# Kernel tuning notes

Measured on AMD Instinct MI355X. Metric: run time of the kernel, lower is better.

The kernel has to match this reference:

```python
import jax, jax.numpy as jnp
import numpy as np
from functools import partial

B, DIN, H, D, HW = 4096, 2048, 1024, 256, 256
MAX_STEPS = 15
STEP = 1.0 / MAX_STEPS
WEIGHT = 1.0


def safe_norm(x):
    # per-sample L2 norm, keepdims, nan-safe at 0
    return jnp.sqrt(jnp.sum(x * x, axis=-1, keepdims=True) + 1e-24)


def setup_inputs() -> dict:
    key = jax.random.key(0)
    ks = jax.random.split(key, 16)
    s = lambda fan: 1.0 / np.sqrt(fan)
    inp = {
        'x_start': jax.random.normal(ks[0], (B, DIN), jnp.float32),
        'x_end': jax.random.normal(ks[1], (B, DIN), jnp.float32),
        'noise_raw': jax.random.normal(ks[2], (B, D), jnp.float32),
        # encoder params
        'W1': jax.random.normal(ks[3], (DIN, H), jnp.float32) * s(DIN),
        'b1': jnp.zeros((H,), jnp.float32),
        'W2': jax.random.normal(ks[4], (H, D), jnp.float32) * s(H),
        'b2': jnp.zeros((D,), jnp.float32),
        # Zermelo wind field params
        'Ww1': jax.random.normal(ks[5], (D, HW), jnp.float32) * s(D),
        'bw1': jnp.zeros((HW,), jnp.float32),
        'Ww2': jax.random.normal(ks[6], (HW, D), jnp.float32) * s(HW),
        'bw2': jnp.zeros((D,), jnp.float32),
        # conformal potential phi params (metric g = exp(phi) I)
        'Wp1': jax.random.normal(ks[7], (D, HW), jnp.float32) * s(D),
        'bp1': jnp.zeros((HW,), jnp.float32),
        'wp2': jax.random.normal(ks[8], (HW,), jnp.float32) * s(HW),
    }
    return inp


def _encode(x, W1, b1, W2, b2):
    return jnp.tanh(x @ W1 + b1) @ W2 + b2  # [B, D]


def _wind(z, Ww1, bw1, Ww2, bw2):
    return jnp.tanh(z @ Ww1 + bw1) @ Ww2 + bw2  # [B, D]


def _grad_phi(x, Wp1, bp1, wp2):
    # phi(x) = wp2 . tanh(x @ Wp1 + bp1); analytic gradient, fully vectorized
    h = jnp.tanh(x @ Wp1 + bp1)          # [B, HW]
    return ((1.0 - h * h) * wp2) @ Wp1.T  # [B, D]


def _accel(x, v, Wp1, bp1, wp2):
    # geodesic spray of conformal metric e^{phi} I:
    # a = -(grad_phi . v) v + 0.5 |v|^2 grad_phi
    g = _grad_phi(x, Wp1, bp1, wp2)
    gv = jnp.sum(g * v, axis=-1, keepdims=True)
    vv = jnp.sum(v * v, axis=-1, keepdims=True)
    return -gv * v + 0.5 * vv * g


def _trace(z0, v0, Wp1, bp1, wp2):
    h = STEP
    acc = partial(_accel, Wp1=Wp1, bp1=bp1, wp2=wp2)

    def step(carry, _):
        x, v = carry
        k1x, k1v = v, acc(x, v)
        k2x, k2v = v + 0.5 * h * k1v, acc(x + 0.5 * h * k1x, v + 0.5 * h * k1v)
        k3x, k3v = v + 0.5 * h * k2v, acc(x + 0.5 * h * k2x, v + 0.5 * h * k2v)
        k4x, k4v = v + h * k3v, acc(x + h * k3x, v + h * k3v)
        xn = x + (h / 6.0) * (k1x + 2 * k2x + 2 * k3x + k4x)
        vn = v + (h / 6.0) * (k1v + 2 * k2v + 2 * k3v + k4v)
        return (xn, vn), xn

    (_, _), xs = jax.lax.scan(step, (z0, v0), None, length=MAX_STEPS)
    return xs  # [MAX_STEPS, B, D] == xs[1:] of the original trace


def reference(x_start, x_end, noise_raw, W1, b1, W2, b2,
              Ww1, bw1, Ww2, bw2, Wp1, bp1, wp2):
    z_s = _encode(x_start, W1, b1, W2, b2)
    z_e = _encode(x_end, W1, b1, W2, b2)
    W_start = _wind(z_s, Ww1, bw1, Ww2, bw2)
    # degenerate-wind fallback: tiny tangent noise (Euclidean manifold -> identity projection)
    noise = noise_raw / (safe_norm(noise_raw) + 1e-12) * 1e-4
    w_norm = safe_norm(W_start)  # [B, 1]
    W_start = jnp.where(w_norm < 1e-5, W_start + noise, W_start)
    xs = _trace(z_s, W_start, Wp1, bp1, wp2)          # [S, B, D]
    dists_sq = jnp.sum((xs - z_e) ** 2, axis=-1)      # [S, B]
    min_dist_sq = jnp.min(dists_sq, axis=0)           # closest approach per sample
    return jnp.mean(min_dist_sq) * WEIGHT
```

## Files before the change

### kernel.cpp

```cpp
#include <hip/hip_runtime.h>
#include <math.h>

typedef short bf8 __attribute__((ext_vector_type(8)));
typedef float f32x4 __attribute__((ext_vector_type(4)));

namespace {

constexpr float H_STEP = 1.0f / 15.0f;

__device__ inline short f2bf(float f) {
  unsigned u = __float_as_uint(f);
  u += 0x7fffu + ((u >> 16) & 1u);
  return (short)(u >> 16);
}

__device__ inline float fast_tanh(float x) {
  const float ax = fabsf(x);
  const float e = __expf(-2.0f * ax);
  const float t = (1.0f - e) * __builtin_amdgcn_rcpf(1.0f + e);
  return copysignf(t, x);
}

__device__ inline float wave_sum(float v) {
#pragma unroll
  for (int sh = 32; sh > 0; sh >>= 1) v += __shfl_xor(v, sh);
  return v;
}

template <int CTRL>
__device__ inline float dppadd(float v) {
  return v + __int_as_float(__builtin_amdgcn_update_dpp(
                 0, __float_as_int(v), CTRL, 0xF, 0xF, true));
}
__device__ inline float red16(float v) {
  v = dppadd<0x121>(v);
  v = dppadd<0x122>(v);
  v = dppadd<0x124>(v);
  v = dppadd<0x128>(v);
  return v;
}

__device__ inline void async16(const void* g, void* l) {
  __builtin_amdgcn_global_load_lds((__attribute__((address_space(1))) void*)g,
                                   (__attribute__((address_space(3))) void*)l,
                                   16, 0, 0);
}


__global__ __launch_bounds__(256) void cvt2(const float* __restrict__ a,
                                            const float* __restrict__ b,
                                            short* __restrict__ dst, long n) {
  const long half = n >> 1;
  long i = ((long)blockIdx.x * 256 + threadIdx.x) * 4;
  const long stride = (long)gridDim.x * 1024;
  for (; i < n; i += stride) {
    const float* s = (i < half) ? (a + i) : (b + (i - half));
    const float4 f = *(const float4*)s;
    ushort4 o;
    o.x = (unsigned short)f2bf(f.x);
    o.y = (unsigned short)f2bf(f.y);
    o.z = (unsigned short)f2bf(f.z);
    o.w = (unsigned short)f2bf(f.w);
    *(ushort4*)(dst + i) = o;
  }
}

__global__ __launch_bounds__(256) void cvt_t(const float* __restrict__ src,
                                             short* __restrict__ dst, int K,
                                             int N) {
  __shared__ float tile[32][33];
  const int k0 = blockIdx.y * 32, n0 = blockIdx.x * 32;
  const int tr = threadIdx.x >> 5, tc = threadIdx.x & 31;
#pragma unroll
  for (int i = 0; i < 32; i += 8)
    tile[tr + i][tc] = src[(size_t)(k0 + tr + i) * N + n0 + tc];
  __syncthreads();
#pragma unroll
  for (int i = 0; i < 32; i += 8)
    dst[(size_t)(n0 + tr + i) * K + k0 + tc] = f2bf(tile[tc][tr + i]);
}

__global__ __launch_bounds__(256) void cvt4(const float* __restrict__ Ww1,
                                            const float* __restrict__ Ww2,
                                            const float* __restrict__ Wp1,
                                            short* __restrict__ d0,
                                            short* __restrict__ d1,
                                            short* __restrict__ d2,
                                            short* __restrict__ d3) {
  __shared__ float tile[32][33];
  const int z = blockIdx.z;
  const int k0 = blockIdx.y * 32, n0 = blockIdx.x * 32;
  const int tr = threadIdx.x >> 5, tc = threadIdx.x & 31;
  if (z == 3) {
#pragma unroll
    for (int i = 0; i < 32; i += 8) {
      const size_t o = (size_t)(k0 + tr + i) * 256 + n0 + tc;
      d3[o] = f2bf(Wp1[o]);
    }
    return;
  }
  const float* src = (z == 0) ? Ww1 : (z == 1) ? Ww2 : Wp1;
  short* dst = (z == 0) ? d0 : (z == 1) ? d1 : d2;
#pragma unroll
  for (int i = 0; i < 32; i += 8)
    tile[tr + i][tc] = src[(size_t)(k0 + tr + i) * 256 + n0 + tc];
  __syncthreads();
#pragma unroll
  for (int i = 0; i < 32; i += 8)
    dst[(size_t)(n0 + tr + i) * 256 + k0 + tc] = f2bf(tile[tc][tr + i]);
}


enum { EPI_TANH = 0, EPI_F32 = 1, EPI_ENC2 = 2 };

template <int EPI>
__global__ __launch_bounds__(256) void gemm128(
    const short* __restrict__ A, const short* __restrict__ Bt,
    const float* __restrict__ bias, float* __restrict__ Cf,
    short* __restrict__ Cb, int M, int N, int K) {
  __shared__ __align__(16) short As[128 * 32];
  __shared__ __align__(16) short Bs[128 * 32];
  const int tid = threadIdx.x;
  const int w = tid >> 6, lane = tid & 63, q = lane >> 4, l15 = lane & 15;
  const int wm = (w >> 1) * 64, wn = (w & 1) * 64;
  const int m0 = blockIdx.y * 128, n0 = blockIdx.x * 128;
  const f32x4 fzero = {0.0f, 0.0f, 0.0f, 0.0f};
  f32x4 acc[4][4];
#pragma unroll
  for (int mt = 0; mt < 4; ++mt)
#pragma unroll
    for (int nt = 0; nt < 4; ++nt) acc[mt][nt] = fzero;

  for (int k0 = 0; k0 < K; k0 += 32) {
#pragma unroll
    for (int j = 0; j < 2; ++j) {
      const int c = w * 128 + j * 64 + lane;
      async16(A + (size_t)(m0 + (c >> 2)) * K + k0 + (c & 3) * 8,
              &As[(w * 128 + j * 64) * 8]);
      async16(Bt + (size_t)(n0 + (c >> 2)) * K + k0 + (c & 3) * 8,
              &Bs[(w * 128 + j * 64) * 8]);
    }
    __syncthreads();
    bf8 af[4], bfr[4];
#pragma unroll
    for (int mt = 0; mt < 4; ++mt)
      af[mt] = *(const bf8*)&As[(wm + mt * 16 + l15) * 32 + q * 8];
#pragma unroll
    for (int nt = 0; nt < 4; ++nt)
      bfr[nt] = *(const bf8*)&Bs[(wn + nt * 16 + l15) * 32 + q * 8];
#pragma unroll
    for (int mt = 0; mt < 4; ++mt)
#pragma unroll
      for (int nt = 0; nt < 4; ++nt)
        acc[mt][nt] = __builtin_amdgcn_mfma_f32_16x16x32_bf16(
            af[mt], bfr[nt], acc[mt][nt], 0, 0, 0);
    __syncthreads();
  }
#pragma unroll
  for (int mt = 0; mt < 4; ++mt)
#pragma unroll
    for (int nt = 0; nt < 4; ++nt) {
      const int col = n0 + wn + nt * 16 + l15;
      const float bcol = bias[col];
#pragma unroll
      for (int rg = 0; rg < 4; ++rg) {
        const int row = m0 + wm + mt * 16 + q * 4 + rg;
        const float val = acc[mt][nt][rg] + bcol;
        if constexpr (EPI == EPI_TANH) {
          Cb[(size_t)row * N + col] = f2bf(fast_tanh(val));
        } else {
          Cf[(size_t)row * N + col] = val;
        }
      }
    }
}

template <int EPI>
__global__ __launch_bounds__(256) void gemm64(
    const short* __restrict__ A, const short* __restrict__ Bt,
    const float* __restrict__ bias, float* __restrict__ Cf,
    short* __restrict__ Cb, float* __restrict__ Cf2, int M, int N, int K) {
  __shared__ __align__(16) short As[64 * 32];
  __shared__ __align__(16) short Bs[64 * 32];
  const int tid = threadIdx.x;
  const int w = tid >> 6, lane = tid & 63, q = lane >> 4, l15 = lane & 15;
  const int wm = (w >> 1) * 32, wn = (w & 1) * 32;
  const int m0 = blockIdx.y * 64, n0 = blockIdx.x * 64;
  const f32x4 fzero = {0.0f, 0.0f, 0.0f, 0.0f};
  f32x4 acc[2][2];
#pragma unroll
  for (int mt = 0; mt < 2; ++mt)
#pragma unroll
    for (int nt = 0; nt < 2; ++nt) acc[mt][nt] = fzero;

  for (int k0 = 0; k0 < K; k0 += 32) {
    const int c = w * 64 + lane;
    async16(A + (size_t)(m0 + (c >> 2)) * K + k0 + (c & 3) * 8,
            &As[(w * 64) * 8]);
    async16(Bt + (size_t)(n0 + (c >> 2)) * K + k0 + (c & 3) * 8,
            &Bs[(w * 64) * 8]);
    __syncthreads();
    bf8 af[2], bfr[2];
#pragma unroll
    for (int mt = 0; mt < 2; ++mt)
      af[mt] = *(const bf8*)&As[(wm + mt * 16 + l15) * 32 + q * 8];
#pragma unroll
    for (int nt = 0; nt < 2; ++nt)
      bfr[nt] = *(const bf8*)&Bs[(wn + nt * 16 + l15) * 32 + q * 8];
#pragma unroll
    for (int mt = 0; mt < 2; ++mt)
#pragma unroll
      for (int nt = 0; nt < 2; ++nt)
        acc[mt][nt] = __builtin_amdgcn_mfma_f32_16x16x32_bf16(
            af[mt], bfr[nt], acc[mt][nt], 0, 0, 0);
    __syncthreads();
  }
#pragma unroll
  for (int mt = 0; mt < 2; ++mt)
#pragma unroll
    for (int nt = 0; nt < 2; ++nt) {
      const int col = n0 + wn + nt * 16 + l15;
      const float bcol = bias[col];
#pragma unroll
      for (int rg = 0; rg < 4; ++rg) {
        const int row = m0 + wm + mt * 16 + q * 4 + rg;
        const float val = acc[mt][nt][rg] + bcol;
        if constexpr (EPI == EPI_TANH) {
          Cb[(size_t)row * N + col] = f2bf(fast_tanh(val));
        } else if constexpr (EPI == EPI_F32) {
          Cf[(size_t)row * N + col] = val;
        } else {
          if (row < 4096) {
            Cf[(size_t)row * N + col] = val;
            Cb[(size_t)row * N + col] = f2bf(val);
          } else {
            Cf2[(size_t)(row - 4096) * N + col] = val;
          }
        }
      }
    }
}


__global__ __launch_bounds__(256) void init_fb(float* __restrict__ V,
                                               const float* __restrict__ nr) {
  const int row = blockIdx.x * 4 + (threadIdx.x >> 6);
  const int lane = threadIdx.x & 63;
  const size_t off = (size_t)row * 256 + (lane << 2);
  float4 wv = *(const float4*)(V + off);
  float s = wv.x * wv.x + wv.y * wv.y + wv.z * wv.z + wv.w * wv.w;
  s = wave_sum(s);
  const float wn = sqrtf(s + 1e-24f);
  if (wn < 1e-5f) {
    const float4 n4 = *(const float4*)(nr + off);
    float ns = n4.x * n4.x + n4.y * n4.y + n4.z * n4.z + n4.w * n4.w;
    ns = wave_sum(ns);
    const float nn = sqrtf(ns + 1e-24f);
    const float sc = 1e-4f / (nn + 1e-12f);
    wv.x += sc * n4.x; wv.y += sc * n4.y; wv.z += sc * n4.z; wv.w += sc * n4.w;
    *(float4*)(V + off) = wv;
  }
}


__global__ __launch_bounds__(512, 2) void trace_fused(
    const float* __restrict__ Xg, const float* __restrict__ Vg,
    const float* __restrict__ ZEg, const short* __restrict__ WT,
    const short* __restrict__ Wp1b, const float* __restrict__ bp1,
    const float* __restrict__ wp2, float* __restrict__ out) {
  constexpr float hs = H_STEP;
  __shared__ __align__(16) short XsL[4096];
  __shared__ __align__(16) short UL[4096];
  __shared__ __align__(16) float gvb[2][16];
  __shared__ __align__(16) float vvb[2][16];
  __shared__ __align__(16) float db[2][16];
  const int tid = threadIdx.x;
  const int w = tid >> 6, lane = tid & 63, q = lane >> 4, l15 = lane & 15;
  const int r0 = blockIdx.x * 16, rb = q * 4;

  if (tid < 16) {
    gvb[0][tid] = 0.0f; gvb[1][tid] = 0.0f;
    vvb[0][tid] = 0.0f; vvb[1][tid] = 0.0f;
    db[0][tid] = 0.0f;  db[1][tid] = 0.0f;
  }

  bf8 B1f[2][8], B2f[2][8];
  int wadr[2][4], radr[8];
  float bp1c[2], wp2c[2];
  float x[2][4], v[2][4], ap[2][4], xacc[2][4], vacc[2][4], ze[2][4], md[4];
#pragma unroll
  for (int t = 0; t < 2; ++t) {
    const int c = w * 32 + t * 16 + l15;
    const int kc = c >> 3, cx = kc & 15, cl = c & 7;
#pragma unroll
    for (int ks = 0; ks < 8; ++ks) {
      B1f[t][ks] = *(const bf8*)(WT + c * 256 + ks * 32 + q * 8);
      B2f[t][ks] = *(const bf8*)(Wp1b + c * 256 + ks * 32 + q * 8);
    }
    bp1c[t] = bp1[c];
    wp2c[t] = wp2[c];
#pragma unroll
    for (int rg = 0; rg < 4; ++rg) {
      wadr[t][rg] = kc * 128 + ((rb + rg) ^ cx) * 8 + cl;
      const size_t off = (size_t)(r0 + rb + rg) * 256 + c;
      x[t][rg] = Xg[off];
      v[t][rg] = Vg[off];
      ze[t][rg] = ZEg[off];
      ap[t][rg] = 0.0f;
      xacc[t][rg] = 0.0f;
      vacc[t][rg] = 0.0f;
    }
  }
#pragma unroll
  for (int ks = 0; ks < 8; ++ks) {
    const int kq = ks * 4 + q;
    radr[ks] = (kq * 16 + (l15 ^ (kq & 15))) * 8;
  }
#pragma unroll
  for (int rg = 0; rg < 4; ++rg) md[rg] = 3.4e38f;
  const f32x4 fzero = {0.0f, 0.0f, 0.0f, 0.0f};
  const float cxv_t[4] = {0.0f, 0.5f * hs, 0.5f * hs, hs};
  const float cxa_t[4] = {0.0f, 0.0f, 0.25f * hs * hs, 0.5f * hs * hs};
  const float cva_t[4] = {0.0f, 0.5f * hs, 0.5f * hs, hs};

#pragma unroll 1
  for (int step = 0; step < 15; ++step) {
#pragma unroll
    for (int st = 0; st < 4; ++st) {
      const int p = st & 1;
      const float cxv = cxv_t[st], cxa = cxa_t[st], cva = cva_t[st];
#pragma unroll
      for (int t = 0; t < 2; ++t)
#pragma unroll
        for (int rg = 0; rg < 4; ++rg)
          XsL[wadr[t][rg]] =
              f2bf(x[t][rg] + cxv * v[t][rg] + cxa * ap[t][rg]);
      __syncthreads();
      bf8 af[8];
#pragma unroll
      for (int ks = 0; ks < 8; ++ks) af[ks] = *(const bf8*)&XsL[radr[ks]];
      f32x4 acc[2];
#pragma unroll
      for (int t = 0; t < 2; ++t) {
        f32x4 a0 = fzero, a1 = fzero;
#pragma unroll
        for (int ks = 0; ks < 8; ks += 2) {
          a0 = __builtin_amdgcn_mfma_f32_16x16x32_bf16(af[ks], B1f[t][ks], a0,
                                                       0, 0, 0);
          a1 = __builtin_amdgcn_mfma_f32_16x16x32_bf16(af[ks + 1],
                                                       B1f[t][ks + 1], a1, 0,
                                                       0, 0);
        }
        acc[t] = a0 + a1;
      }
#pragma unroll
      for (int t = 0; t < 2; ++t)
#pragma unroll
        for (int rg = 0; rg < 4; ++rg) {
          const float th = fast_tanh(acc[t][rg] + bp1c[t]);
          UL[wadr[t][rg]] = f2bf((1.0f - th * th) * wp2c[t]);
        }
      if (tid < 16) {
        gvb[p ^ 1][tid] = 0.0f;
        vvb[p ^ 1][tid] = 0.0f;
      }
      __syncthreads();
#pragma unroll
      for (int ks = 0; ks < 8; ++ks) af[ks] = *(const bf8*)&UL[radr[ks]];
#pragma unroll
      for (int t = 0; t < 2; ++t) {
        f32x4 a0 = fzero, a1 = fzero;
#pragma unroll
        for (int ks = 0; ks < 8; ks += 2) {
          a0 = __builtin_amdgcn_mfma_f32_16x16x32_bf16(af[ks], B2f[t][ks], a0,
                                                       0, 0, 0);
          a1 = __builtin_amdgcn_mfma_f32_16x16x32_bf16(af[ks + 1],
                                                       B2f[t][ks + 1], a1, 0,
                                                       0, 0);
        }
        acc[t] = a0 + a1;
      }
      float pg[4] = {0, 0, 0, 0}, pv[4] = {0, 0, 0, 0};
#pragma unroll
      for (int t = 0; t < 2; ++t)
#pragma unroll
        for (int rg = 0; rg < 4; ++rg) {
          const float vs = fmaf(cva, ap[t][rg], v[t][rg]);
          pg[rg] = fmaf(acc[t][rg], vs, pg[rg]);
          pv[rg] = fmaf(vs, vs, pv[rg]);
        }
#pragma unroll
      for (int rg = 0; rg < 4; ++rg) {
        pg[rg] = red16(pg[rg]);
        pv[rg] = red16(pv[rg]);
      }
      if (l15 == 0) {
#pragma unroll
        for (int rg = 0; rg < 4; ++rg) {
          atomicAdd(&gvb[p][rb + rg], pg[rg]);
          atomicAdd(&vvb[p][rb + rg], pv[rg]);
        }
      }
      __syncthreads();
      const f32x4 gv4 = *(const f32x4*)&gvb[p][rb];
      const f32x4 vv4 = *(const f32x4*)&vvb[p][rb];
#pragma unroll
      for (int t = 0; t < 2; ++t)
#pragma unroll
        for (int rg = 0; rg < 4; ++rg) {
          const float vs = fmaf(cva, ap[t][rg], v[t][rg]);
          const float a = -gv4[rg] * vs + 0.5f * vv4[rg] * acc[t][rg];
          ap[t][rg] = a;
          if (st == 0) {
            xacc[t][rg] = a;
            vacc[t][rg] = a;
          } else if (st < 3) {
            xacc[t][rg] += a;
            vacc[t][rg] += 2.0f * a;
          } else {
            vacc[t][rg] += a;
          }
        }
      if (st == 3) {
        const int sp = step & 1;
        float pd[4] = {0, 0, 0, 0};
#pragma unroll
        for (int t = 0; t < 2; ++t)
#pragma unroll
          for (int rg = 0; rg < 4; ++rg) {
            const float xn =
                x[t][rg] + hs * v[t][rg] + (hs * hs / 6.0f) * xacc[t][rg];
            const float vn = v[t][rg] + (hs / 6.0f) * vacc[t][rg];
            x[t][rg] = xn;
            v[t][rg] = vn;
            const float d = xn - ze[t][rg];
            pd[rg] = fmaf(d, d, pd[rg]);
          }
#pragma unroll
        for (int rg = 0; rg < 4; ++rg) pd[rg] = red16(pd[rg]);
        if (l15 == 0) {
#pragma unroll
          for (int rg = 0; rg < 4; ++rg) atomicAdd(&db[sp][rb + rg], pd[rg]);
        }
        if (tid < 16) db[sp ^ 1][tid] = 0.0f;
        __syncthreads();
        const f32x4 d4 = *(const f32x4*)&db[sp][rb];
#pragma unroll
        for (int rg = 0; rg < 4; ++rg) md[rg] = fminf(md[rg], d4[rg]);
      }
    }
  }
  if (w == 0 && l15 == 0)
    atomicAdd(out, (md[0] + md[1] + md[2] + md[3]) * (1.0f / 4096.0f));
}

}

extern "C" void kernel_launch(void* const* d_in, const int* in_sizes, int n_in,
                              void* d_out, int out_size, void* d_ws,
                              size_t ws_size, hipStream_t stream) {
  (void)in_sizes; (void)n_in; (void)out_size; (void)ws_size;
  const float* x_start = (const float*)d_in[0];
  const float* x_end = (const float*)d_in[1];
  const float* noise = (const float*)d_in[2];
  const float* W1 = (const float*)d_in[3];
  const float* b1 = (const float*)d_in[4];
  const float* W2 = (const float*)d_in[5];
  const float* b2 = (const float*)d_in[6];
  const float* Ww1 = (const float*)d_in[7];
  const float* bw1 = (const float*)d_in[8];
  const float* Ww2 = (const float*)d_in[9];
  const float* bw2 = (const float*)d_in[10];
  const float* Wp1 = (const float*)d_in[11];
  const float* bp1 = (const float*)d_in[12];
  const float* wp2 = (const float*)d_in[13];
  float* out = (float*)d_out;

  float* Xf = (float*)d_ws;
  float* ZEf = Xf + (size_t)4096 * 256;
  float* Vf = ZEf + (size_t)4096 * 256;
  short* Xb = (short*)(Vf + (size_t)4096 * 256);
  short* HWb = Xb + (size_t)4096 * 256;
  short* XSb = HWb + (size_t)4096 * 256;
  short* H1b = XSb + (size_t)8192 * 2048;
  short* W1T = H1b + (size_t)8192 * 1024;
  short* W2T = W1T + (size_t)1024 * 2048;
  short* Ww1T = W2T + (size_t)256 * 1024;
  short* Ww2T = Ww1T + 65536;
  short* WpT = Ww2T + 65536;
  short* Wp1b = WpT + 65536;

  const dim3 blk(256);

  cvt_t<<<dim3(32, 64), blk, 0, stream>>>(W1, W1T, 2048, 1024);
  cvt_t<<<dim3(8, 32), blk, 0, stream>>>(W2, W2T, 1024, 256);
  cvt4<<<dim3(8, 8, 4), blk, 0, stream>>>(Ww1, Ww2, Wp1, Ww1T, Ww2T, WpT,
                                          Wp1b);
  cvt2<<<2048, blk, 0, stream>>>(x_start, x_end, XSb, (long)8192 * 2048);
  gemm128<EPI_TANH><<<dim3(8, 64), blk, 0, stream>>>(
      XSb, W1T, b1, nullptr, H1b, 8192, 1024, 2048);
  gemm64<EPI_ENC2><<<dim3(4, 128), blk, 0, stream>>>(
      H1b, W2T, b2, Xf, Xb, ZEf, 8192, 256, 1024);
  gemm64<EPI_TANH><<<dim3(4, 64), blk, 0, stream>>>(
      Xb, Ww1T, bw1, nullptr, HWb, nullptr, 4096, 256, 256);
  gemm64<EPI_F32><<<dim3(4, 64), blk, 0, stream>>>(
      HWb, Ww2T, bw2, Vf, nullptr, nullptr, 4096, 256, 256);
  init_fb<<<1024, blk, 0, stream>>>(Vf, noise);

  hipMemsetAsync(d_out, 0, sizeof(float), stream);
  trace_fused<<<256, dim3(512), 0, stream>>>(Xf, Vf, ZEf, WpT, Wp1b, bp1, wp2,
                                             out);
}
```

Baseline: 346.0 us.

## Widen trace kernel to 1024 threads, deepen GEMM K-tile, use sech2

The fused RK4 trace kernel now runs 16 waves per block, each owning one 16-column slice instead of two. This halves per-thread register state and raises the number of waves available to hide latency. The large encoder GEMM now loads two 32-wide K chunks per barrier pair, which halves the synchronisation count but doubles shared memory use. tanh-derivative is computed directly as sech^2 via one exp and one rcp. The risks are higher barrier cost across 1024 threads and register pressure under the new launch bounds.

```diff
diff --git a/kernel.cpp b/kernel.cpp
--- a/kernel.cpp
+++ b/kernel.cpp
@@ -19,6 +19,12 @@
   const float e = __expf(-2.0f * ax);
   const float t = (1.0f - e) * __builtin_amdgcn_rcpf(1.0f + e);
   return copysignf(t, x);
+}
+
+__device__ inline float sech2(float x) {
+  const float e = __expf(-2.0f * fabsf(x));
+  const float r = __builtin_amdgcn_rcpf(1.0f + e);
+  return 4.0f * e * r * r;
 }
 
 __device__ inline float wave_sum(float v) {
@@ -118,8 +124,8 @@
     const short* __restrict__ A, const short* __restrict__ Bt,
     const float* __restrict__ bias, float* __restrict__ Cf,
     short* __restrict__ Cb, int M, int N, int K) {
-  __shared__ __align__(16) short As[128 * 32];
-  __shared__ __align__(16) short Bs[128 * 32];
+  __shared__ __align__(16) short As[2 * 128 * 32];
+  __shared__ __align__(16) short Bs[2 * 128 * 32];
   const int tid = threadIdx.x;
   const int w = tid >> 6, lane = tid & 63, q = lane >> 4, l15 = lane & 15;
   const int wm = (w >> 1) * 64, wn = (w & 1) * 64;
@@ -131,29 +137,36 @@
 #pragma unroll
     for (int nt = 0; nt < 4; ++nt) acc[mt][nt] = fzero;
 
-  for (int k0 = 0; k0 < K; k0 += 32) {
-#pragma unroll
-    for (int j = 0; j < 2; ++j) {
-      const int c = w * 128 + j * 64 + lane;
-      async16(A + (size_t)(m0 + (c >> 2)) * K + k0 + (c & 3) * 8,
-              &As[(w * 128 + j * 64) * 8]);
-      async16(Bt + (size_t)(n0 + (c >> 2)) * K + k0 + (c & 3) * 8,
-              &Bs[(w * 128 + j * 64) * 8]);
-    }
+  for (int k0 = 0; k0 < K; k0 += 64) {
+#pragma unroll
+    for (int kcb = 0; kcb < 2; ++kcb)
+#pragma unroll
+      for (int j = 0; j < 2; ++j) {
+        const int c = w * 128 + j * 64 + lane;
+        async16(A + (size_t)(m0 + (c >> 2)) * K + k0 + kcb * 32 + (c & 3) * 8,
+                &As[kcb * 4096 + (w * 128 + j * 64) * 8]);
+        async16(Bt + (size_t)(n0 + (c >> 2)) * K + k0 + kcb * 32 + (c & 3) * 8,
+                &Bs[kcb * 4096 + (w * 128 + j * 64) * 8]);
+      }
     __syncthreads();
-    bf8 af[4], bfr[4];
-#pragma unroll
-    for (int mt = 0; mt < 4; ++mt)
-      af[mt] = *(const bf8*)&As[(wm + mt * 16 + l15) * 32 + q * 8];
-#pragma unroll
-    for (int nt = 0; nt < 4; ++nt)
-      bfr[nt] = *(const bf8*)&Bs[(wn + nt * 16 + l15) * 32 + q * 8];
-#pragma unroll
-    for (int mt = 0; mt < 4; ++mt)
+#pragma unroll
+    for (int kcb = 0; kcb < 2; ++kcb) {
+      bf8 af[4], bfr[4];
+#pragma unroll
+      for (int mt = 0; mt < 4; ++mt)
+        af[mt] =
+            *(const bf8*)&As[kcb * 4096 + (wm + mt * 16 + l15) * 32 + q * 8];
 #pragma unroll
       for (int nt = 0; nt < 4; ++nt)
-        acc[mt][nt] = __builtin_amdgcn_mfma_f32_16x16x32_bf16(
-            af[mt], bfr[nt], acc[mt][nt], 0, 0, 0);
+        bfr[nt] =
+            *(const bf8*)&Bs[kcb * 4096 + (wn + nt * 16 + l15) * 32 + q * 8];
+#pragma unroll
+      for (int mt = 0; mt < 4; ++mt)
+#pragma unroll
+        for (int nt = 0; nt < 4; ++nt)
+          acc[mt][nt] = __builtin_amdgcn_mfma_f32_16x16x32_bf16(
+              af[mt], bfr[nt], acc[mt][nt], 0, 0, 0);
+    }
     __syncthreads();
   }
 #pragma unroll
@@ -263,7 +276,7 @@
 }
 
 
-__global__ __launch_bounds__(512, 2) void trace_fused(
+__global__ __launch_bounds__(1024, 4) void trace_fused(
     const float* __restrict__ Xg, const float* __restrict__ Vg,
     const float* __restrict__ ZEg, const short* __restrict__ WT,
     const short* __restrict__ Wp1b, const float* __restrict__ bp1,
@@ -284,40 +297,39 @@
     db[0][tid] = 0.0f;  db[1][tid] = 0.0f;
   }
 
-  bf8 B1f[2][8], B2f[2][8];
-  int wadr[2][4], radr[8];
-  float bp1c[2], wp2c[2];
-  float x[2][4], v[2][4], ap[2][4], xacc[2][4], vacc[2][4], ze[2][4], md[4];
-#pragma unroll
-  for (int t = 0; t < 2; ++t) {
-    const int c = w * 32 + t * 16 + l15;
+  const int c = w * 16 + l15;
+  bf8 B1f[8], B2f[8];
+#pragma unroll
+  for (int ks = 0; ks < 8; ++ks) {
+    B1f[ks] = *(const bf8*)(WT + c * 256 + ks * 32 + q * 8);
+    B2f[ks] = *(const bf8*)(Wp1b + c * 256 + ks * 32 + q * 8);
+  }
+  const float bp1c = bp1[c];
+  const float wp2c = wp2[c];
+  int wadr[4], radr[8];
+  {
     const int kc = c >> 3, cx = kc & 15, cl = c & 7;
 #pragma unroll
+    for (int rg = 0; rg < 4; ++rg)
+      wadr[rg] = kc * 128 + ((rb + rg) ^ cx) * 8 + cl;
+#pragma unroll
     for (int ks = 0; ks < 8; ++ks) {
-      B1f[t][ks] = *(const bf8*)(WT + c * 256 + ks * 32 + q * 8);
-      B2f[t][ks] = *(const bf8*)(Wp1b + c * 256 + ks * 32 + q * 8);
-    }
-    bp1c[t] = bp1[c];
-    wp2c[t] = wp2[c];
-#pragma unroll
-    for (int rg = 0; rg < 4; ++rg) {
-      wadr[t][rg] = kc * 128 + ((rb + rg) ^ cx) * 8 + cl;
-      const size_t off = (size_t)(r0 + rb + rg) * 256 + c;
-      x[t][rg] = Xg[off];
-      v[t][rg] = Vg[off];
-      ze[t][rg] = ZEg[off];
-      ap[t][rg] = 0.0f;
-      xacc[t][rg] = 0.0f;
-      vacc[t][rg] = 0.0f;
-    }
-  }
-#pragma unroll
-  for (int ks = 0; ks < 8; ++ks) {
-    const int kq = ks * 4 + q;
-    radr[ks] = (kq * 16 + (l15 ^ (kq & 15))) * 8;
-  }
-#pragma unroll
-  for (int rg = 0; rg < 4; ++rg) md[rg] = 3.4e38f;
+      const int kq = ks * 4 + q;
+      radr[ks] = (kq * 16 + (l15 ^ (kq & 15))) * 8;
+    }
+  }
+  float x[4], v[4], ap[4], xacc[4], vacc[4], ze[4], md[4];
+#pragma unroll
+  for (int rg = 0; rg < 4; ++rg) {
+    const size_t off = (size_t)(r0 + rb + rg) * 256 + c;
+    x[rg] = Xg[off];
+    v[rg] = Vg[off];
+    ze[rg] = ZEg[off];
+    ap[rg] = 0.0f;
+    xacc[rg] = 0.0f;
+    vacc[rg] = 0.0f;
+    md[rg] = 3.4e38f;
+  }
   const f32x4 fzero = {0.0f, 0.0f, 0.0f, 0.0f};
   const float cxv_t[4] = {0.0f, 0.5f * hs, 0.5f * hs, hs};
   const float cxa_t[4] = {0.0f, 0.0f, 0.25f * hs * hs, 0.5f * hs * hs};
@@ -330,69 +342,50 @@
       const int p = st & 1;
       const float cxv = cxv_t[st], cxa = cxa_t[st], cva = cva_t[st];
 #pragma unroll
-      for (int t = 0; t < 2; ++t)
-#pragma unroll
-        for (int rg = 0; rg < 4; ++rg)
-          XsL[wadr[t][rg]] =
-              f2bf(x[t][rg] + cxv * v[t][rg] + cxa * ap[t][rg]);
+      for (int rg = 0; rg < 4; ++rg)
+        XsL[wadr[rg]] = f2bf(x[rg] + cxv * v[rg] + cxa * ap[rg]);
       __syncthreads();
-      bf8 af[8];
-#pragma unroll
-      for (int ks = 0; ks < 8; ++ks) af[ks] = *(const bf8*)&XsL[radr[ks]];
-      f32x4 acc[2];
-#pragma unroll
-      for (int t = 0; t < 2; ++t) {
+      f32x4 acc;
+      {
         f32x4 a0 = fzero, a1 = fzero;
 #pragma unroll
         for (int ks = 0; ks < 8; ks += 2) {
-          a0 = __builtin_amdgcn_mfma_f32_16x16x32_bf16(af[ks], B1f[t][ks], a0,
-                                                       0, 0, 0);
-          a1 = __builtin_amdgcn_mfma_f32_16x16x32_bf16(af[ks + 1],
-                                                       B1f[t][ks + 1], a1, 0,
+          const bf8 f0 = *(const bf8*)&XsL[radr[ks]];
+          const bf8 f1 = *(const bf8*)&XsL[radr[ks + 1]];
+          a0 = __builtin_amdgcn_mfma_f32_16x16x32_bf16(f0, B1f[ks], a0, 0, 0,
+                                                       0);
+          a1 = __builtin_amdgcn_mfma_f32_16x16x32_bf16(f1, B1f[ks + 1], a1, 0,
                                                        0, 0);
         }
-        acc[t] = a0 + a1;
-      }
-#pragma unroll
-      for (int t = 0; t < 2; ++t)
-#pragma unroll
-        for (int rg = 0; rg < 4; ++rg) {
-          const float th = fast_tanh(acc[t][rg] + bp1c[t]);
-          UL[wadr[t][rg]] = f2bf((1.0f - th * th) * wp2c[t]);
-        }
+        acc = a0 + a1;
+      }
+#pragma unroll
+      for (int rg = 0; rg < 4; ++rg)
+        UL[wadr[rg]] = f2bf(sech2(acc[rg] + bp1c) * wp2c);
       if (tid < 16) {
         gvb[p ^ 1][tid] = 0.0f;
         vvb[p ^ 1][tid] = 0.0f;
       }
       __syncthreads();
-#pragma unroll
-      for (int ks = 0; ks < 8; ++ks) af[ks] = *(const bf8*)&UL[radr[ks]];
-#pragma unroll
-      for (int t = 0; t < 2; ++t) {
+      {
         f32x4 a0 = fzero, a1 = fzero;
 #pragma unroll
         for (int ks = 0; ks < 8; ks += 2) {
-          a0 = __builtin_amdgcn_mfma_f32_16x16x32_bf16(af[ks], B2f[t][ks], a0,
-                                                       0, 0, 0);
-          a1 = __builtin_amdgcn_mfma_f32_16x16x32_bf16(af[ks + 1],
-                                                       B2f[t][ks + 1], a1, 0,
+          const bf8 f0 = *(const bf8*)&UL[radr[ks]];
+          const bf8 f1 = *(const bf8*)&UL[radr[ks + 1]];
+          a0 = __builtin_amdgcn_mfma_f32_16x16x32_bf16(f0, B2f[ks], a0, 0, 0,
+                                                       0);
+          a1 = __builtin_amdgcn_mfma_f32_16x16x32_bf16(f1, B2f[ks + 1], a1, 0,
                                                        0, 0);
         }
-        acc[t] = a0 + a1;
-      }
-      float pg[4] = {0, 0, 0, 0}, pv[4] = {0, 0, 0, 0};
-#pragma unroll
-      for (int t = 0; t < 2; ++t)
-#pragma unroll
-        for (int rg = 0; rg < 4; ++rg) {
-          const float vs = fmaf(cva, ap[t][rg], v[t][rg]);
-          pg[rg] = fmaf(acc[t][rg], vs, pg[rg]);
-          pv[rg] = fmaf(vs, vs, pv[rg]);
-        }
+        acc = a0 + a1;
+      }
+      float pg[4], pv[4];
 #pragma unroll
       for (int rg = 0; rg < 4; ++rg) {
-        pg[rg] = red16(pg[rg]);
-        pv[rg] = red16(pv[rg]);
+        const float vs = fmaf(cva, ap[rg], v[rg]);
+        pg[rg] = red16(acc[rg] * vs);
+        pv[rg] = red16(vs * vs);
       }
       if (l15 == 0) {
 #pragma unroll
@@ -405,39 +398,32 @@
       const f32x4 gv4 = *(const f32x4*)&gvb[p][rb];
       const f32x4 vv4 = *(const f32x4*)&vvb[p][rb];
 #pragma unroll
-      for (int t = 0; t < 2; ++t)
-#pragma unroll
-        for (int rg = 0; rg < 4; ++rg) {
-          const float vs = fmaf(cva, ap[t][rg], v[t][rg]);
-          const float a = -gv4[rg] * vs + 0.5f * vv4[rg] * acc[t][rg];
-          ap[t][rg] = a;
-          if (st == 0) {
-            xacc[t][rg] = a;
-            vacc[t][rg] = a;
-          } else if (st < 3) {
-            xacc[t][rg] += a;
-            vacc[t][rg] += 2.0f * a;
-          } else {
-            vacc[t][rg] += a;
-          }
-        }
+      for (int rg = 0; rg < 4; ++rg) {
+        const float vs = fmaf(cva, ap[rg], v[rg]);
+        const float a = -gv4[rg] * vs + 0.5f * vv4[rg] * acc[rg];
+        ap[rg] = a;
+        if (st == 0) {
+          xacc[rg] = a;
+          vacc[rg] = a;
+        } else if (st < 3) {
+          xacc[rg] += a;
+          vacc[rg] += 2.0f * a;
+        } else {
+          vacc[rg] += a;
+        }
+      }
       if (st == 3) {
         const int sp = step & 1;
-        float pd[4] = {0, 0, 0, 0};
-#pragma unroll
-        for (int t = 0; t < 2; ++t)
-#pragma unroll
-          for (int rg = 0; rg < 4; ++rg) {
-            const float xn =
-                x[t][rg] + hs * v[t][rg] + (hs * hs / 6.0f) * xacc[t][rg];
-            const float vn = v[t][rg] + (hs / 6.0f) * vacc[t][rg];
-            x[t][rg] = xn;
-            v[t][rg] = vn;
-            const float d = xn - ze[t][rg];
-            pd[rg] = fmaf(d, d, pd[rg]);
-          }
-#pragma unroll
-        for (int rg = 0; rg < 4; ++rg) pd[rg] = red16(pd[rg]);
+        float pd[4];
+#pragma unroll
+        for (int rg = 0; rg < 4; ++rg) {
+          const float xn = x[rg] + hs * v[rg] + (hs * hs / 6.0f) * xacc[rg];
+          const float vn = v[rg] + (hs / 6.0f) * vacc[rg];
+          x[rg] = xn;
+          v[rg] = vn;
+          const float d = xn - ze[rg];
+          pd[rg] = red16(d * d);
+        }
         if (l15 == 0) {
 #pragma unroll
           for (int rg = 0; rg < 4; ++rg) atomicAdd(&db[sp][rb + rg], pd[rg]);
@@ -508,6 +494,6 @@
   init_fb<<<1024, blk, 0, stream>>>(Vf, noise);
 
   hipMemsetAsync(d_out, 0, sizeof(float), stream);
-  trace_fused<<<256, dim3(512), 0, stream>>>(Xf, Vf, ZEf, WpT, Wp1b, bp1, wp2,
-                                             out);
-}
+  trace_fused<<<256, dim3(1024), 0, stream>>>(Xf, Vf, ZEf, WpT, Wp1b, bp1,
+                                              wp2, out);
+}
```

Result: slower. 381.8 us (+10.4%).

## Fuse wind MLP and fallback into trace kernel, merge weight conversions

Applied to the files above, without the earlier changes.

Moves the wind-field MLP (two small GEMMs) and the degenerate-wind noise fallback into the trace kernel, dropping three launches and the round trips of the bf16 Xb, HWb and V intermediates. All weight conversions are merged into one launch, and wp2 is folded into the bf16 Wp1 copy so the spray uses sech² directly. The big encoder GEMM now stages two K-chunks per barrier, halving its synchronisations. The catch is more register pressure and serial startup work inside the trace kernel, plus a larger LDS footprint in the GEMM.

```diff
diff --git a/kernel.cpp b/kernel.cpp
--- a/kernel.cpp
+++ b/kernel.cpp
@@ -19,6 +19,12 @@
   const float e = __expf(-2.0f * ax);
   const float t = (1.0f - e) * __builtin_amdgcn_rcpf(1.0f + e);
   return copysignf(t, x);
+}
+
+__device__ inline float sech2(float x) {
+  const float e = __expf(-2.0f * fabsf(x));
+  const float r = __builtin_amdgcn_rcpf(1.0f + e);
+  return 4.0f * e * r * r;
 }
 
 __device__ inline float wave_sum(float v) {
@@ -65,12 +71,40 @@
   }
 }
 
-__global__ __launch_bounds__(256) void cvt_t(const float* __restrict__ src,
-                                             short* __restrict__ dst, int K,
-                                             int N) {
+__global__ __launch_bounds__(256) void cvt_w(
+    const float* __restrict__ W1, const float* __restrict__ W2,
+    const float* __restrict__ Ww1, const float* __restrict__ Ww2,
+    const float* __restrict__ Wp1, const float* __restrict__ wp2,
+    short* __restrict__ W1T, short* __restrict__ W2T,
+    short* __restrict__ Ww1T, short* __restrict__ Ww2T,
+    short* __restrict__ WpT, short* __restrict__ Wp1s) {
   __shared__ float tile[32][33];
-  const int k0 = blockIdx.y * 32, n0 = blockIdx.x * 32;
+  const int id = blockIdx.x;
   const int tr = threadIdx.x >> 5, tc = threadIdx.x & 31;
+  const float* src;
+  short* dst;
+  int K, N, kt, nt;
+  if (id < 2048) {
+    src = W1; dst = W1T; K = 2048; N = 1024; kt = id >> 5; nt = id & 31;
+  } else if (id < 2304) {
+    src = W2; dst = W2T; K = 1024; N = 256; kt = (id - 2048) >> 3; nt = (id - 2048) & 7;
+  } else if (id < 2368) {
+    src = Ww1; dst = Ww1T; K = 256; N = 256; kt = (id - 2304) >> 3; nt = (id - 2304) & 7;
+  } else if (id < 2432) {
+    src = Ww2; dst = Ww2T; K = 256; N = 256; kt = (id - 2368) >> 3; nt = (id - 2368) & 7;
+  } else if (id < 2496) {
+    src = Wp1; dst = WpT; K = 256; N = 256; kt = (id - 2432) >> 3; nt = (id - 2432) & 7;
+  } else {
+    const int lid = id - 2496;
+    const int k0 = (lid >> 3) * 32, n0 = (lid & 7) * 32;
+#pragma unroll
+    for (int i = 0; i < 32; i += 8) {
+      const size_t o = (size_t)(k0 + tr + i) * 256 + n0 + tc;
+      Wp1s[o] = f2bf(Wp1[o] * wp2[n0 + tc]);
+    }
+    return;
+  }
+  const int k0 = kt * 32, n0 = nt * 32;
 #pragma unroll
   for (int i = 0; i < 32; i += 8)
     tile[tr + i][tc] = src[(size_t)(k0 + tr + i) * N + n0 + tc];
@@ -80,46 +114,13 @@
     dst[(size_t)(n0 + tr + i) * K + k0 + tc] = f2bf(tile[tc][tr + i]);
 }
 
-__global__ __launch_bounds__(256) void cvt4(const float* __restrict__ Ww1,
-                                            const float* __restrict__ Ww2,
-                                            const float* __restrict__ Wp1,
-                                            short* __restrict__ d0,
-                                            short* __restrict__ d1,
-                                            short* __restrict__ d2,
-                                            short* __restrict__ d3) {
-  __shared__ float tile[32][33];
-  const int z = blockIdx.z;
-  const int k0 = blockIdx.y * 32, n0 = blockIdx.x * 32;
-  const int tr = threadIdx.x >> 5, tc = threadIdx.x & 31;
-  if (z == 3) {
-#pragma unroll
-    for (int i = 0; i < 32; i += 8) {
-      const size_t o = (size_t)(k0 + tr + i) * 256 + n0 + tc;
-      d3[o] = f2bf(Wp1[o]);
-    }
-    return;
-  }
-  const float* src = (z == 0) ? Ww1 : (z == 1) ? Ww2 : Wp1;
-  short* dst = (z == 0) ? d0 : (z == 1) ? d1 : d2;
-#pragma unroll
-  for (int i = 0; i < 32; i += 8)
-    tile[tr + i][tc] = src[(size_t)(k0 + tr + i) * 256 + n0 + tc];
-  __syncthreads();
-#pragma unroll
-  for (int i = 0; i < 32; i += 8)
-    dst[(size_t)(n0 + tr + i) * 256 + k0 + tc] = f2bf(tile[tc][tr + i]);
-}
-
-
-enum { EPI_TANH = 0, EPI_F32 = 1, EPI_ENC2 = 2 };
-
-template <int EPI>
-__global__ __launch_bounds__(256) void gemm128(
+
+__global__ __launch_bounds__(256) void gemm128_tanh(
     const short* __restrict__ A, const short* __restrict__ Bt,
-    const float* __restrict__ bias, float* __restrict__ Cf,
-    short* __restrict__ Cb, int M, int N, int K) {
-  __shared__ __align__(16) short As[128 * 32];
-  __shared__ __align__(16) short Bs[128 * 32];
+    const float* __restrict__ bias, short* __restrict__ Cb, int M, int N,
+    int K) {
+  __shared__ __align__(16) short As[2 * 128 * 32];
+  __shared__ __align__(16) short Bs[2 * 128 * 32];
   const int tid = threadIdx.x;
   const int w = tid >> 6, lane = tid & 63, q = lane >> 4, l15 = lane & 15;
   const int wm = (w >> 1) * 64, wn = (w & 1) * 64;
@@ -131,29 +132,36 @@
 #pragma unroll
     for (int nt = 0; nt < 4; ++nt) acc[mt][nt] = fzero;
 
-  for (int k0 = 0; k0 < K; k0 += 32) {
-#pragma unroll
-    for (int j = 0; j < 2; ++j) {
-      const int c = w * 128 + j * 64 + lane;
-      async16(A + (size_t)(m0 + (c >> 2)) * K + k0 + (c & 3) * 8,
-              &As[(w * 128 + j * 64) * 8]);
-      async16(Bt + (size_t)(n0 + (c >> 2)) * K + k0 + (c & 3) * 8,
-              &Bs[(w * 128 + j * 64) * 8]);
-    }
-    __syncthreads();
-    bf8 af[4], bfr[4];
-#pragma unroll
-    for (int mt = 0; mt < 4; ++mt)
-      af[mt] = *(const bf8*)&As[(wm + mt * 16 + l15) * 32 + q * 8];
-#pragma unroll
-    for (int nt = 0; nt < 4; ++nt)
-      bfr[nt] = *(const bf8*)&Bs[(wn + nt * 16 + l15) * 32 + q * 8];
-#pragma unroll
-    for (int mt = 0; mt < 4; ++mt)
+  for (int k0 = 0; k0 < K; k0 += 64) {
+#pragma unroll
+    for (int kcb = 0; kcb < 2; ++kcb)
+#pragma unroll
+      for (int j = 0; j < 2; ++j) {
+        const int c = w * 128 + j * 64 + lane;
+        async16(A + (size_t)(m0 + (c >> 2)) * K + k0 + kcb * 32 + (c & 3) * 8,
+                &As[kcb * 4096 + (w * 128 + j * 64) * 8]);
+        async16(Bt + (size_t)(n0 + (c >> 2)) * K + k0 + kcb * 32 + (c & 3) * 8,
+                &Bs[kcb * 4096 + (w * 128 + j * 64) * 8]);
+      }
+    __syncthreads();
+#pragma unroll
+    for (int kcb = 0; kcb < 2; ++kcb) {
+      bf8 af[4], bfr[4];
+#pragma unroll
+      for (int mt = 0; mt < 4; ++mt)
+        af[mt] =
+            *(const bf8*)&As[kcb * 4096 + (wm + mt * 16 + l15) * 32 + q * 8];
 #pragma unroll
       for (int nt = 0; nt < 4; ++nt)
-        acc[mt][nt] = __builtin_amdgcn_mfma_f32_16x16x32_bf16(
-            af[mt], bfr[nt], acc[mt][nt], 0, 0, 0);
+        bfr[nt] =
+            *(const bf8*)&Bs[kcb * 4096 + (wn + nt * 16 + l15) * 32 + q * 8];
+#pragma unroll
+      for (int mt = 0; mt < 4; ++mt)
+#pragma unroll
+        for (int nt = 0; nt < 4; ++nt)
+          acc[mt][nt] = __builtin_amdgcn_mfma_f32_16x16x32_bf16(
+              af[mt], bfr[nt], acc[mt][nt], 0, 0, 0);
+    }
     __syncthreads();
   }
 #pragma unroll
@@ -165,21 +173,15 @@
 #pragma unroll
       for (int rg = 0; rg < 4; ++rg) {
         const int row = m0 + wm + mt * 16 + q * 4 + rg;
-        const float val = acc[mt][nt][rg] + bcol;
-        if constexpr (EPI == EPI_TANH) {
-          Cb[(size_t)row * N + col] = f2bf(fast_tanh(val));
-        } else {
-          Cf[(size_t)row * N + col] = val;
-        }
-      }
-    }
-}
-
-template <int EPI>
-__global__ __launch_bounds__(256) void gemm64(
+        Cb[(size_t)row * N + col] = f2bf(fast_tanh(acc[mt][nt][rg] + bcol));
+      }
+    }
+}
+
+__global__ __launch_bounds__(256) void gemm64_enc2(
     const short* __restrict__ A, const short* __restrict__ Bt,
-    const float* __restrict__ bias, float* __restrict__ Cf,
-    short* __restrict__ Cb, float* __restrict__ Cf2, int M, int N, int K) {
+    const float* __restrict__ bias, float* __restrict__ Zs,
+    float* __restrict__ Ze, int M, int N, int K) {
   __shared__ __align__(16) short As[64 * 32];
   __shared__ __align__(16) short Bs[64 * 32];
   const int tid = threadIdx.x;
@@ -225,49 +227,22 @@
       for (int rg = 0; rg < 4; ++rg) {
         const int row = m0 + wm + mt * 16 + q * 4 + rg;
         const float val = acc[mt][nt][rg] + bcol;
-        if constexpr (EPI == EPI_TANH) {
-          Cb[(size_t)row * N + col] = f2bf(fast_tanh(val));
-        } else if constexpr (EPI == EPI_F32) {
-          Cf[(size_t)row * N + col] = val;
-        } else {
-          if (row < 4096) {
-            Cf[(size_t)row * N + col] = val;
-            Cb[(size_t)row * N + col] = f2bf(val);
-          } else {
-            Cf2[(size_t)(row - 4096) * N + col] = val;
-          }
-        }
-      }
-    }
-}
-
-
-__global__ __launch_bounds__(256) void init_fb(float* __restrict__ V,
-                                               const float* __restrict__ nr) {
-  const int row = blockIdx.x * 4 + (threadIdx.x >> 6);
-  const int lane = threadIdx.x & 63;
-  const size_t off = (size_t)row * 256 + (lane << 2);
-  float4 wv = *(const float4*)(V + off);
-  float s = wv.x * wv.x + wv.y * wv.y + wv.z * wv.z + wv.w * wv.w;
-  s = wave_sum(s);
-  const float wn = sqrtf(s + 1e-24f);
-  if (wn < 1e-5f) {
-    const float4 n4 = *(const float4*)(nr + off);
-    float ns = n4.x * n4.x + n4.y * n4.y + n4.z * n4.z + n4.w * n4.w;
-    ns = wave_sum(ns);
-    const float nn = sqrtf(ns + 1e-24f);
-    const float sc = 1e-4f / (nn + 1e-12f);
-    wv.x += sc * n4.x; wv.y += sc * n4.y; wv.z += sc * n4.z; wv.w += sc * n4.w;
-    *(float4*)(V + off) = wv;
-  }
+        if (row < 4096)
+          Zs[(size_t)row * N + col] = val;
+        else
+          Ze[(size_t)(row - 4096) * N + col] = val;
+      }
+    }
 }
 
 
 __global__ __launch_bounds__(512, 2) void trace_fused(
-    const float* __restrict__ Xg, const float* __restrict__ Vg,
-    const float* __restrict__ ZEg, const short* __restrict__ WT,
-    const short* __restrict__ Wp1b, const float* __restrict__ bp1,
-    const float* __restrict__ wp2, float* __restrict__ out) {
+    const float* __restrict__ Xg, const float* __restrict__ ZEg,
+    const float* __restrict__ NZg, const short* __restrict__ WT,
+    const short* __restrict__ Wp1s, const short* __restrict__ Ww1T,
+    const short* __restrict__ Ww2T, const float* __restrict__ bw1,
+    const float* __restrict__ bw2, const float* __restrict__ bp1,
+    float* __restrict__ out) {
   constexpr float hs = H_STEP;
   __shared__ __align__(16) short XsL[4096];
   __shared__ __align__(16) short UL[4096];
@@ -284,41 +259,138 @@
     db[0][tid] = 0.0f;  db[1][tid] = 0.0f;
   }
 
-  bf8 B1f[2][8], B2f[2][8];
-  int wadr[2][4], radr[8];
-  float bp1c[2], wp2c[2];
-  float x[2][4], v[2][4], ap[2][4], xacc[2][4], vacc[2][4], ze[2][4], md[4];
+  int cc[2], wadr[2][4], radr[8];
+  float bp1c[2], bw1c[2], bw2c[2];
 #pragma unroll
   for (int t = 0; t < 2; ++t) {
     const int c = w * 32 + t * 16 + l15;
+    cc[t] = c;
     const int kc = c >> 3, cx = kc & 15, cl = c & 7;
 #pragma unroll
-    for (int ks = 0; ks < 8; ++ks) {
-      B1f[t][ks] = *(const bf8*)(WT + c * 256 + ks * 32 + q * 8);
-      B2f[t][ks] = *(const bf8*)(Wp1b + c * 256 + ks * 32 + q * 8);
-    }
+    for (int rg = 0; rg < 4; ++rg)
+      wadr[t][rg] = kc * 128 + ((rb + rg) ^ cx) * 8 + cl;
     bp1c[t] = bp1[c];
-    wp2c[t] = wp2[c];
-#pragma unroll
-    for (int rg = 0; rg < 4; ++rg) {
-      wadr[t][rg] = kc * 128 + ((rb + rg) ^ cx) * 8 + cl;
-      const size_t off = (size_t)(r0 + rb + rg) * 256 + c;
-      x[t][rg] = Xg[off];
-      v[t][rg] = Vg[off];
-      ze[t][rg] = ZEg[off];
-      ap[t][rg] = 0.0f;
-      xacc[t][rg] = 0.0f;
-      vacc[t][rg] = 0.0f;
-    }
+    bw1c[t] = bw1[c];
+    bw2c[t] = bw2[c];
   }
 #pragma unroll
   for (int ks = 0; ks < 8; ++ks) {
     const int kq = ks * 4 + q;
     radr[ks] = (kq * 16 + (l15 ^ (kq & 15))) * 8;
   }
-#pragma unroll
-  for (int rg = 0; rg < 4; ++rg) md[rg] = 3.4e38f;
+  float x[2][4], ze[2][4], nz[2][4];
+#pragma unroll
+  for (int t = 0; t < 2; ++t)
+#pragma unroll
+    for (int rg = 0; rg < 4; ++rg) {
+      const size_t off = (size_t)(r0 + rb + rg) * 256 + cc[t];
+      x[t][rg] = Xg[off];
+      ze[t][rg] = ZEg[off];
+      nz[t][rg] = NZg[off];
+    }
   const f32x4 fzero = {0.0f, 0.0f, 0.0f, 0.0f};
+
+  float v[2][4];
+  {
+    bf8 Wf1[2][8], Wf2[2][8];
+#pragma unroll
+    for (int t = 0; t < 2; ++t)
+#pragma unroll
+      for (int ks = 0; ks < 8; ++ks) {
+        Wf1[t][ks] = *(const bf8*)(Ww1T + cc[t] * 256 + ks * 32 + q * 8);
+        Wf2[t][ks] = *(const bf8*)(Ww2T + cc[t] * 256 + ks * 32 + q * 8);
+      }
+#pragma unroll
+    for (int t = 0; t < 2; ++t)
+#pragma unroll
+      for (int rg = 0; rg < 4; ++rg) XsL[wadr[t][rg]] = f2bf(x[t][rg]);
+    __syncthreads();
+    bf8 af[8];
+#pragma unroll
+    for (int ks = 0; ks < 8; ++ks) af[ks] = *(const bf8*)&XsL[radr[ks]];
+    f32x4 acc[2];
+#pragma unroll
+    for (int t = 0; t < 2; ++t) {
+      f32x4 a0 = fzero, a1 = fzero;
+#pragma unroll
+      for (int ks = 0; ks < 8; ks += 2) {
+        a0 = __builtin_amdgcn_mfma_f32_16x16x32_bf16(af[ks], Wf1[t][ks], a0,
+                                                     0, 0, 0);
+        a1 = __builtin_amdgcn_mfma_f32_16x16x32_bf16(af[ks + 1],
+                                                     Wf1[t][ks + 1], a1, 0, 0,
+                                                     0);
+      }
+      acc[t] = a0 + a1;
+    }
+#pragma unroll
+    for (int t = 0; t < 2; ++t)
+#pragma unroll
+      for (int rg = 0; rg < 4; ++rg)
+        UL[wadr[t][rg]] = f2bf(fast_tanh(acc[t][rg] + bw1c[t]));
+    __syncthreads();
+#pragma unroll
+    for (int ks = 0; ks < 8; ++ks) af[ks] = *(const bf8*)&UL[radr[ks]];
+#pragma unroll
+    for (int t = 0; t < 2; ++t) {
+      f32x4 a0 = fzero, a1 = fzero;
+#pragma unroll
+      for (int ks = 0; ks < 8; ks += 2) {
+        a0 = __builtin_amdgcn_mfma_f32_16x16x32_bf16(af[ks], Wf2[t][ks], a0,
+                                                     0, 0, 0);
+        a1 = __builtin_amdgcn_mfma_f32_16x16x32_bf16(af[ks + 1],
+                                                     Wf2[t][ks + 1], a1, 0, 0,
+                                                     0);
+      }
+      acc[t] = a0 + a1;
+#pragma unroll
+      for (int rg = 0; rg < 4; ++rg) v[t][rg] = acc[t][rg] + bw2c[t];
+    }
+    float pn[4], pm[4];
+#pragma unroll
+    for (int rg = 0; rg < 4; ++rg) {
+      pn[rg] = red16(v[0][rg] * v[0][rg] + v[1][rg] * v[1][rg]);
+      pm[rg] = red16(nz[0][rg] * nz[0][rg] + nz[1][rg] * nz[1][rg]);
+    }
+    if (l15 == 0) {
+#pragma unroll
+      for (int rg = 0; rg < 4; ++rg) {
+        atomicAdd(&gvb[0][rb + rg], pn[rg]);
+        atomicAdd(&vvb[0][rb + rg], pm[rg]);
+      }
+    }
+    __syncthreads();
+#pragma unroll
+    for (int rg = 0; rg < 4; ++rg) {
+      const float wn = sqrtf(gvb[0][rb + rg] + 1e-24f);
+      const float sc = (wn < 1e-5f)
+                           ? 1e-4f / (sqrtf(vvb[0][rb + rg] + 1e-24f) + 1e-12f)
+                           : 0.0f;
+      v[0][rg] = fmaf(sc, nz[0][rg], v[0][rg]);
+      v[1][rg] = fmaf(sc, nz[1][rg], v[1][rg]);
+    }
+    __syncthreads();
+    if (tid < 16) {
+      gvb[0][tid] = 0.0f;
+      vvb[0][tid] = 0.0f;
+    }
+  }
+
+  bf8 B1f[2][8], B2f[2][8];
+#pragma unroll
+  for (int t = 0; t < 2; ++t)
+#pragma unroll
+    for (int ks = 0; ks < 8; ++ks) {
+      B1f[t][ks] = *(const bf8*)(WT + cc[t] * 256 + ks * 32 + q * 8);
+      B2f[t][ks] = *(const bf8*)(Wp1s + cc[t] * 256 + ks * 32 + q * 8);
+    }
+  float ap[2][4], xacc[2][4], vacc[2][4], md[4];
+#pragma unroll
+  for (int rg = 0; rg < 4; ++rg) {
+    ap[0][rg] = 0.0f; ap[1][rg] = 0.0f;
+    xacc[0][rg] = 0.0f; xacc[1][rg] = 0.0f;
+    vacc[0][rg] = 0.0f; vacc[1][rg] = 0.0f;
+    md[rg] = 3.4e38f;
+  }
   const float cxv_t[4] = {0.0f, 0.5f * hs, 0.5f * hs, hs};
   const float cxa_t[4] = {0.0f, 0.0f, 0.25f * hs * hs, 0.5f * hs * hs};
   const float cva_t[4] = {0.0f, 0.5f * hs, 0.5f * hs, hs};
@@ -356,10 +428,8 @@
 #pragma unroll
       for (int t = 0; t < 2; ++t)
 #pragma unroll
-        for (int rg = 0; rg < 4; ++rg) {
-          const float th = fast_tanh(acc[t][rg] + bp1c[t]);
-          UL[wadr[t][rg]] = f2bf((1.0f - th * th) * wp2c[t]);
-        }
+        for (int rg = 0; rg < 4; ++rg)
+          UL[wadr[t][rg]] = f2bf(sech2(acc[t][rg] + bp1c[t]));
       if (tid < 16) {
         gvb[p ^ 1][tid] = 0.0f;
         vvb[p ^ 1][tid] = 0.0f;
@@ -380,19 +450,13 @@
         }
         acc[t] = a0 + a1;
       }
-      float pg[4] = {0, 0, 0, 0}, pv[4] = {0, 0, 0, 0};
-#pragma unroll
-      for (int t = 0; t < 2; ++t)
-#pragma unroll
-        for (int rg = 0; rg < 4; ++rg) {
-          const float vs = fmaf(cva, ap[t][rg], v[t][rg]);
-          pg[rg] = fmaf(acc[t][rg], vs, pg[rg]);
-          pv[rg] = fmaf(vs, vs, pv[rg]);
-        }
+      float vs[2][4], pg[4], pv[4];
 #pragma unroll
       for (int rg = 0; rg < 4; ++rg) {
-        pg[rg] = red16(pg[rg]);
-        pv[rg] = red16(pv[rg]);
+        vs[0][rg] = fmaf(cva, ap[0][rg], v[0][rg]);
+        vs[1][rg] = fmaf(cva, ap[1][rg], v[1][rg]);
+        pg[rg] = red16(fmaf(acc[0][rg], vs[0][rg], acc[1][rg] * vs[1][rg]));
+        pv[rg] = red16(fmaf(vs[0][rg], vs[0][rg], vs[1][rg] * vs[1][rg]));
       }
       if (l15 == 0) {
 #pragma unroll
@@ -408,8 +472,7 @@
       for (int t = 0; t < 2; ++t)
 #pragma unroll
         for (int rg = 0; rg < 4; ++rg) {
-          const float vs = fmaf(cva, ap[t][rg], v[t][rg]);
-          const float a = -gv4[rg] * vs + 0.5f * vv4[rg] * acc[t][rg];
+          const float a = -gv4[rg] * vs[t][rg] + 0.5f * vv4[rg] * acc[t][rg];
           ap[t][rg] = a;
           if (st == 0) {
             xacc[t][rg] = a;
@@ -423,21 +486,22 @@
         }
       if (st == 3) {
         const int sp = step & 1;
-        float pd[4] = {0, 0, 0, 0};
-#pragma unroll
-        for (int t = 0; t < 2; ++t)
-#pragma unroll
-          for (int rg = 0; rg < 4; ++rg) {
+        float pd[4];
+#pragma unroll
+        for (int rg = 0; rg < 4; ++rg) {
+          float acc_d = 0.0f;
+#pragma unroll
+          for (int t = 0; t < 2; ++t) {
             const float xn =
                 x[t][rg] + hs * v[t][rg] + (hs * hs / 6.0f) * xacc[t][rg];
             const float vn = v[t][rg] + (hs / 6.0f) * vacc[t][rg];
             x[t][rg] = xn;
             v[t][rg] = vn;
             const float d = xn - ze[t][rg];
-            pd[rg] = fmaf(d, d, pd[rg]);
+            acc_d = fmaf(d, d, acc_d);
           }
-#pragma unroll
-        for (int rg = 0; rg < 4; ++rg) pd[rg] = red16(pd[rg]);
+          pd[rg] = red16(acc_d);
+        }
         if (l15 == 0) {
 #pragma unroll
           for (int rg = 0; rg < 4; ++rg) atomicAdd(&db[sp][rb + rg], pd[rg]);
@@ -478,36 +542,25 @@
 
   float* Xf = (float*)d_ws;
   float* ZEf = Xf + (size_t)4096 * 256;
-  float* Vf = ZEf + (size_t)4096 * 256;
-  short* Xb = (short*)(Vf + (size_t)4096 * 256);
-  short* HWb = Xb + (size_t)4096 * 256;
-  short* XSb = HWb + (size_t)4096 * 256;
+  short* XSb = (short*)(ZEf + (size_t)4096 * 256);
   short* H1b = XSb + (size_t)8192 * 2048;
   short* W1T = H1b + (size_t)8192 * 1024;
   short* W2T = W1T + (size_t)1024 * 2048;
   short* Ww1T = W2T + (size_t)256 * 1024;
   short* Ww2T = Ww1T + 65536;
   short* WpT = Ww2T + 65536;
-  short* Wp1b = WpT + 65536;
+  short* Wp1s = WpT + 65536;
 
   const dim3 blk(256);
 
-  cvt_t<<<dim3(32, 64), blk, 0, stream>>>(W1, W1T, 2048, 1024);
-  cvt_t<<<dim3(8, 32), blk, 0, stream>>>(W2, W2T, 1024, 256);
-  cvt4<<<dim3(8, 8, 4), blk, 0, stream>>>(Ww1, Ww2, Wp1, Ww1T, Ww2T, WpT,
-                                          Wp1b);
+  cvt_w<<<2560, blk, 0, stream>>>(W1, W2, Ww1, Ww2, Wp1, wp2, W1T, W2T, Ww1T,
+                                  Ww2T, WpT, Wp1s);
   cvt2<<<2048, blk, 0, stream>>>(x_start, x_end, XSb, (long)8192 * 2048);
-  gemm128<EPI_TANH><<<dim3(8, 64), blk, 0, stream>>>(
-      XSb, W1T, b1, nullptr, H1b, 8192, 1024, 2048);
-  gemm64<EPI_ENC2><<<dim3(4, 128), blk, 0, stream>>>(
-      H1b, W2T, b2, Xf, Xb, ZEf, 8192, 256, 1024);
-  gemm64<EPI_TANH><<<dim3(4, 64), blk, 0, stream>>>(
-      Xb, Ww1T, bw1, nullptr, HWb, nullptr, 4096, 256, 256);
-  gemm64<EPI_F32><<<dim3(4, 64), blk, 0, stream>>>(
-      HWb, Ww2T, bw2, Vf, nullptr, nullptr, 4096, 256, 256);
-  init_fb<<<1024, blk, 0, stream>>>(Vf, noise);
-
+  gemm128_tanh<<<dim3(8, 64), blk, 0, stream>>>(XSb, W1T, b1, H1b, 8192, 1024,
+                                                2048);
+  gemm64_enc2<<<dim3(4, 128), blk, 0, stream>>>(H1b, W2T, b2, Xf, ZEf, 8192,
+                                                256, 1024);
   hipMemsetAsync(d_out, 0, sizeof(float), stream);
-  trace_fused<<<256, dim3(512), 0, stream>>>(Xf, Vf, ZEf, WpT, Wp1b, bp1, wp2,
-                                             out);
-}
+  trace_fused<<<256, dim3(512), 0, stream>>>(Xf, ZEf, noise, WpT, Wp1s, Ww1T,
+                                             Ww2T, bw1, bw2, bp1, out);
+}
```

Result: faster. 325.5 us (-5.9%).
